# Kernel optimization log

Hardware: AMD Instinct MI355X
Metric: run time of the kernel (lower is better)

The kernel has to match this reference:

```python
import jax, jax.numpy as jnp
import numpy as np

B, N, C_IN, C_OUT, K, D_EMB = 32, 4096, 64, 64, 2, 16


def setup_inputs() -> dict:
    key = jax.random.key(0)
    ks = jax.random.split(key, 7)
    x = jax.random.normal(ks[0], (B, N, C_IN), jnp.float32)
    node_embeddings = jax.random.normal(ks[1], (N, D_EMB), jnp.float32)
    weights_pool = jax.random.normal(ks[2], (D_EMB, K, C_IN, C_OUT), jnp.float32) * 0.1
    bias_pool = jax.random.normal(ks[3], (D_EMB, C_OUT), jnp.float32) * 0.1
    lin_w = jax.random.normal(ks[4], (C_OUT, C_IN), jnp.float32) * 0.1
    lin_b = jax.random.normal(ks[5], (C_OUT,), jnp.float32) * 0.1
    adj = jax.random.uniform(ks[6], (N, N), jnp.float32)
    return dict(x=x, node_embeddings=node_embeddings, weights_pool=weights_pool,
                bias_pool=bias_pool, lin_w=lin_w, lin_b=lin_b, adj=adj)


def _sym_norm_adj(W):
    # W + 0.5*I, then D^{-1/2} W D^{-1/2} with D = diag(rowsum)
    n = W.shape[0]
    W = W + 0.5 * jnp.eye(n, dtype=W.dtype)
    sd = jnp.sqrt(1.0 / jnp.sum(W, axis=1))
    return sd[:, None] * W * sd[None, :]


def reference(x, node_embeddings, weights_pool, bias_pool, lin_w, lin_b, adj):
    n = node_embeddings.shape[0]
    # adaptive adjacency: softmax(relu(E E^T)) over neighbors
    supports_dyn = jax.nn.softmax(jax.nn.relu(node_embeddings @ node_embeddings.T), axis=1)
    supports = jnp.stack([jnp.eye(n, dtype=x.dtype), supports_dyn], axis=0)  # [K=2, N, N]
    # node-adaptive weights/bias generated from embeddings
    weights = jnp.einsum('nd,dkio->nkio', node_embeddings, weights_pool)  # [N,K,Cin,Cout]
    bias = node_embeddings @ bias_pool  # [N, Cout]
    # multi-hop aggregation + per-node conv
    x_g = jnp.einsum('knm,bmc->bnkc', supports, x)  # [B,N,K,Cin]
    x_gconv = jnp.einsum('bnki,nkio->bno', x_g, weights) + bias[None]  # [B,N,Cout]
    # static branch: init applies F.softmax(dim=1) to sym-normed adj, forward re-softmaxes dim=-1
    A = jax.nn.softmax(jax.nn.softmax(_sym_norm_adj(adj), axis=1), axis=-1)
    # einsum 'nm,bmc->bmc' == scale node m by sum_n A[n,m]
    scale = jnp.sum(A, axis=0)  # [N]
    x_static = (scale[None, :, None] * x) @ lin_w.T + lin_b  # [B,N,Cout]
    return x_gconv + jax.nn.sigmoid(x_static) * x_static
```

## Files before the change

kernel.cpp:

```cpp
#include <hip/hip_runtime.h>
#include <stdint.h>

#define Bdim 32
#define Ndim 4096
#define Cin  64
#define Cout 64
#define Demb 16

typedef __bf16 bf16x8 __attribute__((ext_vector_type(8)));
typedef float  f32x4  __attribute__((ext_vector_type(4)));

#define GLOBAL_AS(p) ((__attribute__((address_space(1))) void*)(p))
#define LDS_AS(p)    ((__attribute__((address_space(3))) void*)(p))

__device__ __forceinline__ uint16_t f2bf(float x) {
    union { float f; uint32_t u; } v; v.f = x;
    uint32_t r = v.u + 0x7FFFu + ((v.u >> 16) & 1u);
    return (uint16_t)(r >> 16);
}

__device__ __forceinline__ bf16x8 pack8(float4 a, float4 b) {
    union { uint16_t u[8]; bf16x8 v; } r;
    r.u[0] = f2bf(a.x); r.u[1] = f2bf(a.y); r.u[2] = f2bf(a.z); r.u[3] = f2bf(a.w);
    r.u[4] = f2bf(b.x); r.u[5] = f2bf(b.y); r.u[6] = f2bf(b.z); r.u[7] = f2bf(b.w);
    return r.v;
}

__global__ __launch_bounds__(256) void p1_prep(const float* __restrict__ E,
                                               const float* __restrict__ x,
                                               const float* __restrict__ adj,
                                               const float* __restrict__ pool,
                                               uint16_t* __restrict__ A,
                                               float* __restrict__ invA,
                                               uint16_t* __restrict__ Xtt,
                                               float* __restrict__ sd,
                                               float* __restrict__ scale,
                                               float* __restrict__ poolT) {
    __shared__ __align__(16) uint8_t smem[9232];
    const int t = threadIdx.x;
    const int blk = blockIdx.x;

    if (blk < 256) {
        float* Er_s = (float*)smem;
        float* red_s = (float*)(smem + 1024);
        const int n0 = blk * 16;
        Er_s[t] = E[n0 * Demb + t];
        __syncthreads();
        for (int half = 0; half < 2; ++half) {
            float er[8][16];
#pragma unroll
            for (int r = 0; r < 8; ++r)
#pragma unroll
                for (int d = 0; d < 16; ++d) er[r][d] = Er_s[(half * 8 + r) * 16 + d];
            float sacc[8];
#pragma unroll
            for (int r = 0; r < 8; ++r) sacc[r] = 0.f;
            for (int c = 0; c < 16; ++c) {
                const int m = c * 256 + t;
                const float4* ep = (const float4*)(E + (size_t)m * Demb);
                float4 e0 = ep[0], e1 = ep[1], e2 = ep[2], e3 = ep[3];
                float em[16] = {e0.x, e0.y, e0.z, e0.w, e1.x, e1.y, e1.z, e1.w,
                                e2.x, e2.y, e2.z, e2.w, e3.x, e3.y, e3.z, e3.w};
#pragma unroll
                for (int r = 0; r < 8; ++r) {
                    float v = 0.f;
#pragma unroll
                    for (int d = 0; d < 16; ++d) v = fmaf(er[r][d], em[d], v);
                    v = fmaxf(v, 0.f);
                    const float e = __expf(v);
                    sacc[r] += e;
                    A[(size_t)(n0 + half * 8 + r) * Ndim + m] = f2bf(e);
                }
            }
#pragma unroll
            for (int r = 0; r < 8; ++r) {
                float s = sacc[r];
#pragma unroll
                for (int off = 32; off > 0; off >>= 1) s += __shfl_down(s, off, 64);
                __syncthreads();
                if ((t & 63) == 0) red_s[t >> 6] = s;
                __syncthreads();
                if (t == 0)
                    invA[n0 + half * 8 + r] = 1.f / (red_s[0] + red_s[1] + red_s[2] + red_s[3]);
            }
            __syncthreads();
        }
    } else if (blk < 2304) {
        auto T = (uint16_t(*)[72])smem;
        const int idx = blk - 256;
        const int m0 = (idx & 63) * 64;
        const int b = idx >> 6;
        const int c = t & 63;
#pragma unroll
        for (int j = 0; j < 16; ++j) {
            const int m = (t >> 6) + j * 4;
            T[c][m] = f2bf(x[((size_t)b * Ndim + (m0 + m)) * Cin + c]);
        }
        __syncthreads();
        const int c2 = t >> 2, mo = (t & 3) * 16;
        const uint4* src = (const uint4*)&T[c2][mo];
        uint4 v0 = src[0], v1 = src[1];
        uint4* dst = (uint4*)(Xtt + (size_t)(b * Cin + c2) * Ndim + m0 + mo);
        dst[0] = v0;
        dst[1] = v1;
    } else if (blk < 6400) {
        float* red_s = (float*)smem;
        const int n = blk - 2304;
        if (n < 16) scale[n * 256 + t] = 0.f;
        const float4* ap = (const float4*)(adj + (size_t)n * Ndim);
        float s = 0.f;
#pragma unroll
        for (int q = 0; q < 4; ++q) {
            float4 a = ap[q * 256 + t];
            s += a.x + a.y + a.z + a.w;
        }
#pragma unroll
        for (int off = 32; off > 0; off >>= 1) s += __shfl_down(s, off, 64);
        if ((t & 63) == 0) red_s[t >> 6] = s;
        __syncthreads();
        if (t == 0) sd[n] = sqrtf(1.f / (red_s[0] + red_s[1] + red_s[2] + red_s[3] + 0.5f));
    } else {
        const int idx = blk - 6400;
        const int d = idx >> 2;
        const int base = (idx & 3) * 2048;
#pragma unroll
        for (int j = 0; j < 8; ++j) {
            const int e = base + j * 256 + t;
            const float v = pool[d * 8192 + e];
            poolT[d * 8192 + (e & 63) * 128 + (e >> 6)] = v;
        }
    }
}

__device__ __forceinline__ float block_reduce(float v, float* red_s, int t, bool domax) {
#pragma unroll
    for (int off = 32; off > 0; off >>= 1) {
        float o = __shfl_down(v, off, 64);
        v = domax ? fmaxf(v, o) : (v + o);
    }
    __syncthreads();
    if ((t & 63) == 0) red_s[t >> 6] = v;
    __syncthreads();
    return domax ? fmaxf(fmaxf(red_s[0], red_s[1]), fmaxf(red_s[2], red_s[3]))
                 : (red_s[0] + red_s[1] + red_s[2] + red_s[3]);
}

__global__ __launch_bounds__(256) void p2_mid(const float* __restrict__ E,
                                              const float* __restrict__ adj,
                                              const float* __restrict__ sd,
                                              const float* __restrict__ poolT,
                                              const float* __restrict__ bias_pool,
                                              float* __restrict__ scale,
                                              uint16_t* __restrict__ Wt,
                                              float* __restrict__ biasn) {
    __shared__ __align__(16) uint8_t smem[2064];
    const int t = threadIdx.x;
    const int blk = blockIdx.x;

    if (blk < 256) {
        float* red_s = (float*)smem;
        const int nb = blk * 16;
        float sdm[16], colsum[16];
#pragma unroll
        for (int q = 0; q < 4; ++q) {
            float4 v = *(const float4*)(sd + q * 1024 + t * 4);
            sdm[q * 4 + 0] = v.x; sdm[q * 4 + 1] = v.y;
            sdm[q * 4 + 2] = v.z; sdm[q * 4 + 3] = v.w;
            colsum[q * 4 + 0] = colsum[q * 4 + 1] = colsum[q * 4 + 2] = colsum[q * 4 + 3] = 0.f;
        }
        for (int r = 0; r < 16; ++r) {
            const int n = nb + r;
            const float sdn = sd[n];
            float v[16];
#pragma unroll
            for (int q = 0; q < 4; ++q) {
                float4 a = *(const float4*)(adj + (size_t)n * Ndim + q * 1024 + t * 4);
                const int mb = q * 1024 + t * 4;
                v[q * 4 + 0] = a.x + ((mb + 0) == n ? 0.5f : 0.f);
                v[q * 4 + 1] = a.y + ((mb + 1) == n ? 0.5f : 0.f);
                v[q * 4 + 2] = a.z + ((mb + 2) == n ? 0.5f : 0.f);
                v[q * 4 + 3] = a.w + ((mb + 3) == n ? 0.5f : 0.f);
            }
            float mx = -1e30f;
#pragma unroll
            for (int i = 0; i < 16; ++i) { v[i] = sdn * v[i] * sdm[i]; mx = fmaxf(mx, v[i]); }
            mx = block_reduce(mx, red_s, t, true);
            float s1 = 0.f;
#pragma unroll
            for (int i = 0; i < 16; ++i) { v[i] = __expf(v[i] - mx); s1 += v[i]; }
            s1 = block_reduce(s1, red_s, t, false);
            const float inv1 = 1.f / s1;
            float s2 = 0.f;
#pragma unroll
            for (int i = 0; i < 16; ++i) { v[i] = __expf(v[i] * inv1); s2 += v[i]; }
            s2 = block_reduce(s2, red_s, t, false);
            const float inv2 = 1.f / s2;
#pragma unroll
            for (int i = 0; i < 16; ++i) colsum[i] += v[i] * inv2;
        }
#pragma unroll
        for (int q = 0; q < 4; ++q)
#pragma unroll
            for (int u = 0; u < 4; ++u)
                atomicAdd(scale + q * 1024 + t * 4 + u, colsum[q * 4 + u]);
    } else {
        float* En = (float*)smem;
        const int idx = blk - 256;
        const int ec = idx & 7;
        const int n0 = (idx >> 3) * 32;
        En[t] = E[n0 * Demb + t];
        En[t + 256] = E[n0 * Demb + t + 256];
        __syncthreads();

        const int e0 = ec * 1024 + t * 4;
        float4 P[16];
#pragma unroll
        for (int d = 0; d < 16; ++d) P[d] = *(const float4*)(poolT + d * 8192 + e0);

        for (int g = 0; g < 32; ++g) {
            float4 acc = {0.f, 0.f, 0.f, 0.f};
#pragma unroll
            for (int d = 0; d < 16; ++d) {
                const float e = En[g * 16 + d];
                acc.x = fmaf(e, P[d].x, acc.x);
                acc.y = fmaf(e, P[d].y, acc.y);
                acc.z = fmaf(e, P[d].z, acc.z);
                acc.w = fmaf(e, P[d].w, acc.w);
            }
            union { uint16_t u[4]; uint2 v; } r;
            r.u[0] = f2bf(acc.x); r.u[1] = f2bf(acc.y);
            r.u[2] = f2bf(acc.z); r.u[3] = f2bf(acc.w);
            *(uint2*)(Wt + (size_t)(n0 + g) * 8192 + e0) = r.v;
        }

        if (ec == 0) {
            const int o = t & 63, gq = t >> 6;
#pragma unroll
            for (int gi = 0; gi < 8; ++gi) {
                const int g = gi * 4 + gq;
                float a = 0.f;
#pragma unroll
                for (int d = 0; d < 16; ++d) a = fmaf(En[g * 16 + d], bias_pool[d * 64 + o], a);
                biasn[(size_t)(n0 + g) * 64 + o] = a;
            }
        }
    }
}

#define GK 4096
#define GN 2048
__global__ __launch_bounds__(256) void k3_gemm(const uint16_t* __restrict__ Abf,
                                               const uint16_t* __restrict__ Bbf,
                                               const float* __restrict__ invA,
                                               uint16_t* __restrict__ Cbf) {
    __shared__ __align__(16) uint16_t As[128 * 32];
    __shared__ __align__(16) uint16_t Bs[128 * 32];
    const int t = threadIdx.x;
    const int lane = t & 63;
    const int w = t >> 6;
    const int wr = w >> 1, wc = w & 1;
    const int bm = blockIdx.y * 128;
    const int bn = blockIdx.x * 128;

    f32x4 acc[4][4];
#pragma unroll
    for (int i = 0; i < 4; ++i)
#pragma unroll
        for (int j = 0; j < 4; ++j) acc[i][j] = (f32x4){0.f, 0.f, 0.f, 0.f};

    const uint16_t* agp[2];
    const uint16_t* bgp[2];
    uint16_t* alp[2];
    uint16_t* blp[2];
#pragma unroll
    for (int i = 0; i < 2; ++i) {
        const int r = w * 32 + i * 16 + (lane >> 2);
        const int cg = (lane & 3) ^ ((r >> 1) & 3);
        agp[i] = Abf + (size_t)(bm + r) * GK + cg * 8;
        bgp[i] = Bbf + (size_t)(bn + r) * GK + cg * 8;
        alp[i] = &As[(w * 32 + i * 16) * 32];
        blp[i] = &Bs[(w * 32 + i * 16) * 32];
    }

    int offA[4], offB[4];
#pragma unroll
    for (int i = 0; i < 4; ++i) {
        const int m = wr * 64 + i * 16 + (lane & 15);
        offA[i] = m * 32 + (((lane >> 4) ^ ((m >> 1) & 3)) * 8);
        const int n = wc * 64 + i * 16 + (lane & 15);
        offB[i] = n * 32 + (((lane >> 4) ^ ((n >> 1) & 3)) * 8);
    }

    for (int kt = 0; kt < GK / 32; ++kt) {
#pragma unroll
        for (int i = 0; i < 2; ++i) {
            __builtin_amdgcn_global_load_lds(GLOBAL_AS(agp[i] + (size_t)kt * 32), LDS_AS(alp[i]), 16, 0, 0);
            __builtin_amdgcn_global_load_lds(GLOBAL_AS(bgp[i] + (size_t)kt * 32), LDS_AS(blp[i]), 16, 0, 0);
        }
        __syncthreads();
        bf16x8 af[4], bfr[4];
#pragma unroll
        for (int i = 0; i < 4; ++i) {
            af[i] = *(const bf16x8*)(As + offA[i]);
            bfr[i] = *(const bf16x8*)(Bs + offB[i]);
        }
#pragma unroll
        for (int i = 0; i < 4; ++i)
#pragma unroll
            for (int j = 0; j < 4; ++j)
                acc[i][j] = __builtin_amdgcn_mfma_f32_16x16x32_bf16(af[i], bfr[j], acc[i][j], 0, 0, 0);
        __syncthreads();
    }
#pragma unroll
    for (int i = 0; i < 4; ++i) {
        float invv[4];
#pragma unroll
        for (int r = 0; r < 4; ++r)
            invv[r] = invA[bm + wr * 64 + i * 16 + (lane >> 4) * 4 + r];
#pragma unroll
        for (int j = 0; j < 4; ++j)
#pragma unroll
            for (int r = 0; r < 4; ++r) {
                const int row = bm + wr * 64 + i * 16 + (lane >> 4) * 4 + r;
                const int col = bn + wc * 64 + j * 16 + (lane & 15);
                Cbf[(size_t)row * GN + col] = f2bf(acc[i][j][r] * invv[r]);
            }
    }
}

__global__ __launch_bounds__(256) void k6_gconv(const float* __restrict__ x,
                                                const uint16_t* __restrict__ XG,
                                                const uint16_t* __restrict__ Wt,
                                                const float* __restrict__ biasn,
                                                const float* __restrict__ scale,
                                                const float* __restrict__ lin_w,
                                                const float* __restrict__ lin_b,
                                                float* __restrict__ out) {
    __shared__ __align__(16) uint16_t Ws[4][64][136];
    __shared__ __align__(16) uint16_t Lws[64][72];
    const int t = threadIdx.x;
    const int n0 = blockIdx.x * 4;

#pragma unroll
    for (int j = 0; j < 16; ++j) {
        const int e8 = (j * 256 + t) * 8;
        const int g = e8 >> 13;
        const int r = e8 & 8191;
        uint4 v = *(const uint4*)(Wt + (size_t)(n0 + g) * 8192 + r);
        *(uint4*)&Ws[g][r >> 7][r & 127] = v;
    }
    {
        const int o = t >> 2, i0 = (t & 3) * 16;
        const float4* lp = (const float4*)(lin_w + o * 64 + i0);
        float4 a0 = lp[0], a1 = lp[1], a2 = lp[2], a3 = lp[3];
        union { uint16_t u[16]; uint4 v[2]; } r;
        r.u[0] = f2bf(a0.x); r.u[1] = f2bf(a0.y); r.u[2]  = f2bf(a0.z); r.u[3]  = f2bf(a0.w);
        r.u[4] = f2bf(a1.x); r.u[5] = f2bf(a1.y); r.u[6]  = f2bf(a1.z); r.u[7]  = f2bf(a1.w);
        r.u[8] = f2bf(a2.x); r.u[9] = f2bf(a2.y); r.u[10] = f2bf(a2.z); r.u[11] = f2bf(a2.w);
        r.u[12] = f2bf(a3.x); r.u[13] = f2bf(a3.y); r.u[14] = f2bf(a3.z); r.u[15] = f2bf(a3.w);
        *(uint4*)&Lws[o][i0] = r.v[0];
        *(uint4*)&Lws[o][i0 + 8] = r.v[1];
    }

    const int w = t >> 6, lane = t & 63;
    const int n = n0 + w;
    const int l15 = lane & 15;
    const int q8 = (lane >> 4) * 8;

    bf16x8 a[2][4];
#pragma unroll
    for (int mt = 0; mt < 2; ++mt) {
        const int b = mt * 16 + l15;
        const float* xp = x + ((size_t)b * Ndim + n) * 64 + q8;
        a[mt][0] = pack8(((const float4*)xp)[0], ((const float4*)xp)[1]);
        a[mt][1] = pack8(((const float4*)(xp + 32))[0], ((const float4*)(xp + 32))[1]);
        const uint16_t* gp = XG + (size_t)n * 2048 + b * 64 + q8;
        a[mt][2] = *(const bf16x8*)gp;
        a[mt][3] = *(const bf16x8*)(gp + 32);
    }

    f32x4 accg[2][4], accs[2][4];
#pragma unroll
    for (int mt = 0; mt < 2; ++mt)
#pragma unroll
        for (int j = 0; j < 4; ++j) {
            accg[mt][j] = (f32x4){0.f, 0.f, 0.f, 0.f};
            accs[mt][j] = (f32x4){0.f, 0.f, 0.f, 0.f};
        }

    __syncthreads();

#pragma unroll
    for (int ks = 0; ks < 4; ++ks) {
        bf16x8 bw[4];
#pragma unroll
        for (int j = 0; j < 4; ++j)
            bw[j] = *(const bf16x8*)&Ws[w][j * 16 + l15][ks * 32 + q8];
#pragma unroll
        for (int mt = 0; mt < 2; ++mt)
#pragma unroll
            for (int j = 0; j < 4; ++j)
                accg[mt][j] = __builtin_amdgcn_mfma_f32_16x16x32_bf16(a[mt][ks], bw[j], accg[mt][j], 0, 0, 0);
        if (ks < 2) {
            bf16x8 bl[4];
#pragma unroll
            for (int j = 0; j < 4; ++j)
                bl[j] = *(const bf16x8*)&Lws[j * 16 + l15][ks * 32 + q8];
#pragma unroll
            for (int mt = 0; mt < 2; ++mt)
#pragma unroll
                for (int j = 0; j < 4; ++j)
                    accs[mt][j] = __builtin_amdgcn_mfma_f32_16x16x32_bf16(a[mt][ks], bl[j], accs[mt][j], 0, 0, 0);
        }
    }

    const float sc = scale[n];
#pragma unroll
    for (int j = 0; j < 4; ++j) {
        const int o = j * 16 + l15;
        const float bn = biasn[(size_t)n * 64 + o];
        const float lb = lin_b[o];
#pragma unroll
        for (int mt = 0; mt < 2; ++mt)
#pragma unroll
            for (int r = 0; r < 4; ++r) {
                const int b = mt * 16 + (lane >> 4) * 4 + r;
                const float gg = accg[mt][j][r] + bn;
                const float xs = sc * accs[mt][j][r] + lb;
                out[((size_t)b * Ndim + n) * 64 + o] = gg + xs / (1.f + __expf(-xs));
            }
    }
}

extern "C" void kernel_launch(void* const* d_in, const int* in_sizes, int n_in,
                              void* d_out, int out_size, void* d_ws, size_t ws_size,
                              hipStream_t stream) {
    const float* x         = (const float*)d_in[0];
    const float* E         = (const float*)d_in[1];
    const float* pool      = (const float*)d_in[2];
    const float* bias_pool = (const float*)d_in[3];
    const float* lin_w     = (const float*)d_in[4];
    const float* lin_b     = (const float*)d_in[5];
    const float* adj       = (const float*)d_in[6];
    float* out = (float*)d_out;

    uint8_t* ws = (uint8_t*)d_ws;
    uint16_t* A     = (uint16_t*)(ws);
    uint16_t* Xtt   = (uint16_t*)(ws + 33554432);
    uint16_t* XG    = (uint16_t*)(ws + 50331648);
    uint16_t* Wt    = (uint16_t*)(ws + 67108864);
    float*    biasn = (float*)   (ws + 134217728);
    float*    sd    = (float*)   (ws + 135266304);
    float*    scale = (float*)   (ws + 135282688);
    float*    poolT = (float*)   (ws + 135299072);
    float*    invA  = (float*)   (ws + 135823360);

    p1_prep<<<dim3(6464), dim3(256), 0, stream>>>(E, x, adj, pool, A, invA, Xtt, sd, scale, poolT);
    p2_mid<<<dim3(1280), dim3(256), 0, stream>>>(E, adj, sd, poolT, bias_pool, scale, Wt, biasn);
    k3_gemm<<<dim3(16, 32), dim3(256), 0, stream>>>(A, Xtt, invA, XG);
    k6_gconv<<<dim3(1024), dim3(256), 0, stream>>>(x, XG, Wt, biasn, scale, lin_w, lin_b, out);
}
```

Measured before the change: 348.8 us.

## Merge GEMM into mid-stage kernel, drop softmax max pass, load weights directly

Folds the dense bf16 GEMM blocks into the same launch as the static-softmax column-sum and per-node weight generation blocks, so the independent work runs concurrently and one launch is saved. Removes the max-subtraction reduction from the first softmax, relying on the bounded input values to avoid overflow, which saves a block reduction per row. In the final gconv kernel, per-node weights are now read straight from global memory into MFMA operands instead of being staged through shared memory. The trade-offs are a larger shared-memory footprint for every block of the fused kernel, which may reduce occupancy, and possibly less coalesced weight loads.

After: 338.7 us. 1.03x faster.

```diff
diff --git a/kernel.cpp b/kernel.cpp
--- a/kernel.cpp
+++ b/kernel.cpp
@@ -132,34 +132,109 @@
     }
 }
 
-__device__ __forceinline__ float block_reduce(float v, float* red_s, int t, bool domax) {
-#pragma unroll
-    for (int off = 32; off > 0; off >>= 1) {
-        float o = __shfl_down(v, off, 64);
-        v = domax ? fmaxf(v, o) : (v + o);
-    }
+__device__ __forceinline__ float block_reduce_sum(float v, float* red_s, int t) {
+#pragma unroll
+    for (int off = 32; off > 0; off >>= 1) v += __shfl_down(v, off, 64);
     __syncthreads();
     if ((t & 63) == 0) red_s[t >> 6] = v;
     __syncthreads();
-    return domax ? fmaxf(fmaxf(red_s[0], red_s[1]), fmaxf(red_s[2], red_s[3]))
-                 : (red_s[0] + red_s[1] + red_s[2] + red_s[3]);
-}
-
-__global__ __launch_bounds__(256) void p2_mid(const float* __restrict__ E,
-                                              const float* __restrict__ adj,
-                                              const float* __restrict__ sd,
-                                              const float* __restrict__ poolT,
-                                              const float* __restrict__ bias_pool,
-                                              float* __restrict__ scale,
-                                              uint16_t* __restrict__ Wt,
-                                              float* __restrict__ biasn) {
-    __shared__ __align__(16) uint8_t smem[2064];
+    return red_s[0] + red_s[1] + red_s[2] + red_s[3];
+}
+
+#define GK 4096
+#define GN 2048
+__global__ __launch_bounds__(256) void p2_fused(const uint16_t* __restrict__ Abf,
+                                                const uint16_t* __restrict__ Bbf,
+                                                const float* __restrict__ invA,
+                                                uint16_t* __restrict__ Cbf,
+                                                const float* __restrict__ E,
+                                                const float* __restrict__ adj,
+                                                const float* __restrict__ sd,
+                                                const float* __restrict__ poolT,
+                                                const float* __restrict__ bias_pool,
+                                                float* __restrict__ scale,
+                                                uint16_t* __restrict__ Wt,
+                                                float* __restrict__ biasn) {
+    __shared__ __align__(16) uint8_t smem[16384];
     const int t = threadIdx.x;
     const int blk = blockIdx.x;
 
-    if (blk < 256) {
+    if (blk < 512) {
+        uint16_t* As = (uint16_t*)smem;
+        uint16_t* Bs = (uint16_t*)(smem + 8192);
+        const int lane = t & 63;
+        const int w = t >> 6;
+        const int wr = w >> 1, wc = w & 1;
+        const int bm = (blk >> 4) * 128;
+        const int bn = (blk & 15) * 128;
+
+        f32x4 acc[4][4];
+#pragma unroll
+        for (int i = 0; i < 4; ++i)
+#pragma unroll
+            for (int j = 0; j < 4; ++j) acc[i][j] = (f32x4){0.f, 0.f, 0.f, 0.f};
+
+        const uint16_t* agp[2];
+        const uint16_t* bgp[2];
+        uint16_t* alp[2];
+        uint16_t* blp[2];
+#pragma unroll
+        for (int i = 0; i < 2; ++i) {
+            const int r = w * 32 + i * 16 + (lane >> 2);
+            const int cg = (lane & 3) ^ ((r >> 1) & 3);
+            agp[i] = Abf + (size_t)(bm + r) * GK + cg * 8;
+            bgp[i] = Bbf + (size_t)(bn + r) * GK + cg * 8;
+            alp[i] = &As[(w * 32 + i * 16) * 32];
+            blp[i] = &Bs[(w * 32 + i * 16) * 32];
+        }
+
+        int offA[4], offB[4];
+#pragma unroll
+        for (int i = 0; i < 4; ++i) {
+            const int m = wr * 64 + i * 16 + (lane & 15);
+            offA[i] = m * 32 + (((lane >> 4) ^ ((m >> 1) & 3)) * 8);
+            const int n = wc * 64 + i * 16 + (lane & 15);
+            offB[i] = n * 32 + (((lane >> 4) ^ ((n >> 1) & 3)) * 8);
+        }
+
+        for (int kt = 0; kt < GK / 32; ++kt) {
+#pragma unroll
+            for (int i = 0; i < 2; ++i) {
+                __builtin_amdgcn_global_load_lds(GLOBAL_AS(agp[i] + (size_t)kt * 32), LDS_AS(alp[i]), 16, 0, 0);
+                __builtin_amdgcn_global_load_lds(GLOBAL_AS(bgp[i] + (size_t)kt * 32), LDS_AS(blp[i]), 16, 0, 0);
+            }
+            __syncthreads();
+            bf16x8 af[4], bfr[4];
+#pragma unroll
+            for (int i = 0; i < 4; ++i) {
+                af[i] = *(const bf16x8*)(As + offA[i]);
+                bfr[i] = *(const bf16x8*)(Bs + offB[i]);
+            }
+#pragma unroll
+            for (int i = 0; i < 4; ++i)
+#pragma unroll
+                for (int j = 0; j < 4; ++j)
+                    acc[i][j] = __builtin_amdgcn_mfma_f32_16x16x32_bf16(af[i], bfr[j], acc[i][j], 0, 0, 0);
+            __syncthreads();
+        }
+#pragma unroll
+        for (int i = 0; i < 4; ++i) {
+            float invv[4];
+#pragma unroll
+            for (int r = 0; r < 4; ++r)
+                invv[r] = invA[bm + wr * 64 + i * 16 + (lane >> 4) * 4 + r];
+#pragma unroll
+            for (int j = 0; j < 4; ++j)
+#pragma unroll
+                for (int r = 0; r < 4; ++r) {
+                    const int row = bm + wr * 64 + i * 16 + (lane >> 4) * 4 + r;
+                    const int col = bn + wc * 64 + j * 16 + (lane & 15);
+                    Cbf[(size_t)row * GN + col] = f2bf(acc[i][j][r] * invv[r]);
+                }
+        }
+    } else if (blk < 768) {
         float* red_s = (float*)smem;
-        const int nb = blk * 16;
+        const int nb = (blk - 512) * 16;
         float sdm[16], colsum[16];
 #pragma unroll
         for (int q = 0; q < 4; ++q) {
@@ -181,19 +256,15 @@
                 v[q * 4 + 2] = a.z + ((mb + 2) == n ? 0.5f : 0.f);
                 v[q * 4 + 3] = a.w + ((mb + 3) == n ? 0.5f : 0.f);
             }
-            float mx = -1e30f;
-#pragma unroll
-            for (int i = 0; i < 16; ++i) { v[i] = sdn * v[i] * sdm[i]; mx = fmaxf(mx, v[i]); }
-            mx = block_reduce(mx, red_s, t, true);
             float s1 = 0.f;
 #pragma unroll
-            for (int i = 0; i < 16; ++i) { v[i] = __expf(v[i] - mx); s1 += v[i]; }
-            s1 = block_reduce(s1, red_s, t, false);
+            for (int i = 0; i < 16; ++i) { v[i] = __expf(sdn * v[i] * sdm[i]); s1 += v[i]; }
+            s1 = block_reduce_sum(s1, red_s, t);
             const float inv1 = 1.f / s1;
             float s2 = 0.f;
 #pragma unroll
             for (int i = 0; i < 16; ++i) { v[i] = __expf(v[i] * inv1); s2 += v[i]; }
-            s2 = block_reduce(s2, red_s, t, false);
+            s2 = block_reduce_sum(s2, red_s, t);
             const float inv2 = 1.f / s2;
 #pragma unroll
             for (int i = 0; i < 16; ++i) colsum[i] += v[i] * inv2;
@@ -205,7 +276,7 @@
                 atomicAdd(scale + q * 1024 + t * 4 + u, colsum[q * 4 + u]);
     } else {
         float* En = (float*)smem;
-        const int idx = blk - 256;
+        const int idx = blk - 768;
         const int ec = idx & 7;
         const int n0 = (idx >> 3) * 32;
         En[t] = E[n0 * Demb + t];
@@ -244,87 +315,6 @@
                 biasn[(size_t)(n0 + g) * 64 + o] = a;
             }
         }
-    }
-}
-
-#define GK 4096
-#define GN 2048
-__global__ __launch_bounds__(256) void k3_gemm(const uint16_t* __restrict__ Abf,
-                                               const uint16_t* __restrict__ Bbf,
-                                               const float* __restrict__ invA,
-                                               uint16_t* __restrict__ Cbf) {
-    __shared__ __align__(16) uint16_t As[128 * 32];
-    __shared__ __align__(16) uint16_t Bs[128 * 32];
-    const int t = threadIdx.x;
-    const int lane = t & 63;
-    const int w = t >> 6;
-    const int wr = w >> 1, wc = w & 1;
-    const int bm = blockIdx.y * 128;
-    const int bn = blockIdx.x * 128;
-
-    f32x4 acc[4][4];
-#pragma unroll
-    for (int i = 0; i < 4; ++i)
-#pragma unroll
-        for (int j = 0; j < 4; ++j) acc[i][j] = (f32x4){0.f, 0.f, 0.f, 0.f};
-
-    const uint16_t* agp[2];
-    const uint16_t* bgp[2];
-    uint16_t* alp[2];
-    uint16_t* blp[2];
-#pragma unroll
-    for (int i = 0; i < 2; ++i) {
-        const int r = w * 32 + i * 16 + (lane >> 2);
-        const int cg = (lane & 3) ^ ((r >> 1) & 3);
-        agp[i] = Abf + (size_t)(bm + r) * GK + cg * 8;
-        bgp[i] = Bbf + (size_t)(bn + r) * GK + cg * 8;
-        alp[i] = &As[(w * 32 + i * 16) * 32];
-        blp[i] = &Bs[(w * 32 + i * 16) * 32];
-    }
-
-    int offA[4], offB[4];
-#pragma unroll
-    for (int i = 0; i < 4; ++i) {
-        const int m = wr * 64 + i * 16 + (lane & 15);
-        offA[i] = m * 32 + (((lane >> 4) ^ ((m >> 1) & 3)) * 8);
-        const int n = wc * 64 + i * 16 + (lane & 15);
-        offB[i] = n * 32 + (((lane >> 4) ^ ((n >> 1) & 3)) * 8);
-    }
-
-    for (int kt = 0; kt < GK / 32; ++kt) {
-#pragma unroll
-        for (int i = 0; i < 2; ++i) {
-            __builtin_amdgcn_global_load_lds(GLOBAL_AS(agp[i] + (size_t)kt * 32), LDS_AS(alp[i]), 16, 0, 0);
-            __builtin_amdgcn_global_load_lds(GLOBAL_AS(bgp[i] + (size_t)kt * 32), LDS_AS(blp[i]), 16, 0, 0);
-        }
-        __syncthreads();
-        bf16x8 af[4], bfr[4];
-#pragma unroll
-        for (int i = 0; i < 4; ++i) {
-            af[i] = *(const bf16x8*)(As + offA[i]);
-            bfr[i] = *(const bf16x8*)(Bs + offB[i]);
-        }
-#pragma unroll
-        for (int i = 0; i < 4; ++i)
-#pragma unroll
-            for (int j = 0; j < 4; ++j)
-                acc[i][j] = __builtin_amdgcn_mfma_f32_16x16x32_bf16(af[i], bfr[j], acc[i][j], 0, 0, 0);
-        __syncthreads();
-    }
-#pragma unroll
-    for (int i = 0; i < 4; ++i) {
-        float invv[4];
-#pragma unroll
-        for (int r = 0; r < 4; ++r)
-            invv[r] = invA[bm + wr * 64 + i * 16 + (lane >> 4) * 4 + r];
-#pragma unroll
-        for (int j = 0; j < 4; ++j)
-#pragma unroll
-            for (int r = 0; r < 4; ++r) {
-                const int row = bm + wr * 64 + i * 16 + (lane >> 4) * 4 + r;
-                const int col = bn + wc * 64 + j * 16 + (lane & 15);
-                Cbf[(size_t)row * GN + col] = f2bf(acc[i][j][r] * invv[r]);
-            }
     }
 }
 
@@ -336,19 +326,10 @@
                                                 const float* __restrict__ lin_w,
                                                 const float* __restrict__ lin_b,
                                                 float* __restrict__ out) {
-    __shared__ __align__(16) uint16_t Ws[4][64][136];
     __shared__ __align__(16) uint16_t Lws[64][72];
     const int t = threadIdx.x;
     const int n0 = blockIdx.x * 4;
 
-#pragma unroll
-    for (int j = 0; j < 16; ++j) {
-        const int e8 = (j * 256 + t) * 8;
-        const int g = e8 >> 13;
-        const int r = e8 & 8191;
-        uint4 v = *(const uint4*)(Wt + (size_t)(n0 + g) * 8192 + r);
-        *(uint4*)&Ws[g][r >> 7][r & 127] = v;
-    }
     {
         const int o = t >> 2, i0 = (t & 3) * 16;
         const float4* lp = (const float4*)(lin_w + o * 64 + i0);
@@ -388,6 +369,8 @@
             accs[mt][j] = (f32x4){0.f, 0.f, 0.f, 0.f};
         }
 
+    const uint16_t* wp = Wt + (size_t)n * 8192 + l15 * 128 + q8;
+
     __syncthreads();
 
 #pragma unroll
@@ -395,7 +378,7 @@
         bf16x8 bw[4];
 #pragma unroll
         for (int j = 0; j < 4; ++j)
-            bw[j] = *(const bf16x8*)&Ws[w][j * 16 + l15][ks * 32 + q8];
+            bw[j] = *(const bf16x8*)(wp + j * 2048 + ks * 32);
 #pragma unroll
         for (int mt = 0; mt < 2; ++mt)
 #pragma unroll
@@ -456,7 +439,7 @@
     float*    invA  = (float*)   (ws + 135823360);
 
     p1_prep<<<dim3(6464), dim3(256), 0, stream>>>(E, x, adj, pool, A, invA, Xtt, sd, scale, poolT);
-    p2_mid<<<dim3(1280), dim3(256), 0, stream>>>(E, adj, sd, poolT, bias_pool, scale, Wt, biasn);
-    k3_gemm<<<dim3(16, 32), dim3(256), 0, stream>>>(A, Xtt, invA, XG);
+    p2_fused<<<dim3(1792), dim3(256), 0, stream>>>(A, Xtt, invA, XG, E, adj, sd, poolT,
+                                                   bias_pool, scale, Wt, biasn);
     k6_gconv<<<dim3(1024), dim3(256), 0, stream>>>(x, XG, Wt, biasn, scale, lin_w, lin_b, out);
 }
```

## Use per-wave row softmax in adjacency colsum and load gconv weights directly

Applied to the files above, without the earlier changes.

The adjacency column-sum path now gives each wavefront whole rows, so softmax reductions use wave shuffles instead of block-level barriers. The row max subtraction is dropped because the values are bounded, and per-thread column sums are merged through LDS atomics before the global atomics. In the gconv kernel, the per-node weight tile is read straight from global memory into registers rather than staged through LDS, which cuts LDS usage and a copy. The trade-off is much higher register pressure (64-element arrays), dropping max-subtraction relies on the inputs keeping exp in range, and the weight loads become scattered global reads.

Measured after the change: 338.2 us. -3.0%, faster.

```diff
diff --git a/kernel.cpp b/kernel.cpp
--- a/kernel.cpp
+++ b/kernel.cpp
@@ -132,19 +132,6 @@
     }
 }
 
-__device__ __forceinline__ float block_reduce(float v, float* red_s, int t, bool domax) {
-#pragma unroll
-    for (int off = 32; off > 0; off >>= 1) {
-        float o = __shfl_down(v, off, 64);
-        v = domax ? fmaxf(v, o) : (v + o);
-    }
-    __syncthreads();
-    if ((t & 63) == 0) red_s[t >> 6] = v;
-    __syncthreads();
-    return domax ? fmaxf(fmaxf(red_s[0], red_s[1]), fmaxf(red_s[2], red_s[3]))
-                 : (red_s[0] + red_s[1] + red_s[2] + red_s[3]);
-}
-
 __global__ __launch_bounds__(256) void p2_mid(const float* __restrict__ E,
                                               const float* __restrict__ adj,
                                               const float* __restrict__ sd,
@@ -153,56 +140,71 @@
                                               float* __restrict__ scale,
                                               uint16_t* __restrict__ Wt,
                                               float* __restrict__ biasn) {
-    __shared__ __align__(16) uint8_t smem[2064];
+    __shared__ __align__(16) uint8_t smem[16384];
     const int t = threadIdx.x;
     const int blk = blockIdx.x;
 
     if (blk < 256) {
-        float* red_s = (float*)smem;
-        const int nb = blk * 16;
-        float sdm[16], colsum[16];
-#pragma unroll
-        for (int q = 0; q < 4; ++q) {
-            float4 v = *(const float4*)(sd + q * 1024 + t * 4);
-            sdm[q * 4 + 0] = v.x; sdm[q * 4 + 1] = v.y;
-            sdm[q * 4 + 2] = v.z; sdm[q * 4 + 3] = v.w;
-            colsum[q * 4 + 0] = colsum[q * 4 + 1] = colsum[q * 4 + 2] = colsum[q * 4 + 3] = 0.f;
-        }
-        for (int r = 0; r < 16; ++r) {
+        float* cs = (float*)smem;
+#pragma unroll
+        for (int i = 0; i < 16; ++i) cs[i * 256 + t] = 0.f;
+        __syncthreads();
+
+        const int wv = t >> 6, l = t & 63;
+        const int nb = blk * 16 + wv * 4;
+
+        float sdm[64];
+#pragma unroll
+        for (int i = 0; i < 16; ++i) {
+            float4 s4 = *(const float4*)(sd + i * 256 + l * 4);
+            sdm[i * 4 + 0] = s4.x; sdm[i * 4 + 1] = s4.y;
+            sdm[i * 4 + 2] = s4.z; sdm[i * 4 + 3] = s4.w;
+        }
+        float colsum[64];
+#pragma unroll
+        for (int k = 0; k < 64; ++k) colsum[k] = 0.f;
+
+        for (int r = 0; r < 4; ++r) {
             const int n = nb + r;
             const float sdn = sd[n];
-            float v[16];
-#pragma unroll
-            for (int q = 0; q < 4; ++q) {
-                float4 a = *(const float4*)(adj + (size_t)n * Ndim + q * 1024 + t * 4);
-                const int mb = q * 1024 + t * 4;
-                v[q * 4 + 0] = a.x + ((mb + 0) == n ? 0.5f : 0.f);
-                v[q * 4 + 1] = a.y + ((mb + 1) == n ? 0.5f : 0.f);
-                v[q * 4 + 2] = a.z + ((mb + 2) == n ? 0.5f : 0.f);
-                v[q * 4 + 3] = a.w + ((mb + 3) == n ? 0.5f : 0.f);
-            }
-            float mx = -1e30f;
-#pragma unroll
-            for (int i = 0; i < 16; ++i) { v[i] = sdn * v[i] * sdm[i]; mx = fmaxf(mx, v[i]); }
-            mx = block_reduce(mx, red_s, t, true);
+            float e1[64];
             float s1 = 0.f;
 #pragma unroll
-            for (int i = 0; i < 16; ++i) { v[i] = __expf(v[i] - mx); s1 += v[i]; }
-            s1 = block_reduce(s1, red_s, t, false);
+            for (int i = 0; i < 16; ++i) {
+                float4 a4 = *(const float4*)(adj + (size_t)n * Ndim + i * 256 + l * 4);
+                const int c0 = i * 256 + l * 4;
+                float vv[4] = {a4.x, a4.y, a4.z, a4.w};
+#pragma unroll
+                for (int u = 0; u < 4; ++u) {
+                    const float vd = vv[u] + ((c0 + u) == n ? 0.5f : 0.f);
+                    const float e = __expf(sdn * vd * sdm[i * 4 + u]);
+                    e1[i * 4 + u] = e;
+                    s1 += e;
+                }
+            }
+#pragma unroll
+            for (int off = 32; off > 0; off >>= 1) s1 += __shfl_xor(s1, off, 64);
             const float inv1 = 1.f / s1;
             float s2 = 0.f;
 #pragma unroll
-            for (int i = 0; i < 16; ++i) { v[i] = __expf(v[i] * inv1); s2 += v[i]; }
-            s2 = block_reduce(s2, red_s, t, false);
+            for (int k = 0; k < 64; ++k) {
+                const float e = __expf(e1[k] * inv1);
+                e1[k] = e;
+                s2 += e;
+            }
+#pragma unroll
+            for (int off = 32; off > 0; off >>= 1) s2 += __shfl_xor(s2, off, 64);
             const float inv2 = 1.f / s2;
 #pragma unroll
-            for (int i = 0; i < 16; ++i) colsum[i] += v[i] * inv2;
-        }
-#pragma unroll
-        for (int q = 0; q < 4; ++q)
-#pragma unroll
-            for (int u = 0; u < 4; ++u)
-                atomicAdd(scale + q * 1024 + t * 4 + u, colsum[q * 4 + u]);
+            for (int k = 0; k < 64; ++k) colsum[k] = fmaf(e1[k], inv2, colsum[k]);
+        }
+#pragma unroll
+        for (int k = 0; k < 64; ++k)
+            atomicAdd(&cs[(k >> 2) * 256 + l * 4 + (k & 3)], colsum[k]);
+        __syncthreads();
+#pragma unroll
+        for (int i = 0; i < 16; ++i)
+            atomicAdd(scale + i * 256 + t, cs[i * 256 + t]);
     } else {
         float* En = (float*)smem;
         const int idx = blk - 256;
@@ -336,19 +338,10 @@
                                                 const float* __restrict__ lin_w,
                                                 const float* __restrict__ lin_b,
                                                 float* __restrict__ out) {
-    __shared__ __align__(16) uint16_t Ws[4][64][136];
     __shared__ __align__(16) uint16_t Lws[64][72];
     const int t = threadIdx.x;
     const int n0 = blockIdx.x * 4;
 
-#pragma unroll
-    for (int j = 0; j < 16; ++j) {
-        const int e8 = (j * 256 + t) * 8;
-        const int g = e8 >> 13;
-        const int r = e8 & 8191;
-        uint4 v = *(const uint4*)(Wt + (size_t)(n0 + g) * 8192 + r);
-        *(uint4*)&Ws[g][r >> 7][r & 127] = v;
-    }
     {
         const int o = t >> 2, i0 = (t & 3) * 16;
         const float4* lp = (const float4*)(lin_w + o * 64 + i0);
@@ -388,6 +381,8 @@
             accs[mt][j] = (f32x4){0.f, 0.f, 0.f, 0.f};
         }
 
+    const uint16_t* wp = Wt + (size_t)n * 8192 + l15 * 128 + q8;
+
     __syncthreads();
 
 #pragma unroll
@@ -395,7 +390,7 @@
         bf16x8 bw[4];
 #pragma unroll
         for (int j = 0; j < 4; ++j)
-            bw[j] = *(const bf16x8*)&Ws[w][j * 16 + l15][ks * 32 + q8];
+            bw[j] = *(const bf16x8*)(wp + j * 2048 + ks * 32);
 #pragma unroll
         for (int mt = 0; mt < 2; ++mt)
 #pragma unroll
```
